# Optimization experiments

Hardware: AMD Instinct MI355X
Metric: run time of the kernel (lower is better)

## Reference

```python
import jax, jax.numpy as jnp
import numpy as np

B, S, H = 64, 2048, 1024
INPUT_SCALE = 100.0
DT = 0.01


def setup_inputs() -> dict:
    key = jax.random.key(0)
    ks = jax.random.split(key, 16)
    def vec(k, scale=0.5):
        return jax.random.normal(k, (H,), jnp.float32) * scale
    x_codes = 65.0 + 10.0 * jax.random.normal(ks[0], (B, S), jnp.float32)
    return {
        "x_codes": x_codes,
        "Wi_w": vec(ks[1]), "Wi_b": vec(ks[2], 0.1),
        "Wf_w": vec(ks[3]), "Wf_b": vec(ks[4], 0.1),
        "Wo_w": vec(ks[5]), "Wo_b": vec(ks[6], 0.1),
        "Wg_w": vec(ks[7]), "Wg_b": vec(ks[8], 0.1),
        "Wl_w": vec(ks[9]), "Wl_b": vec(ks[10], 0.1),
        "proj_w": jax.random.normal(ks[11], (2, H), jnp.float32) * 0.03,
        "proj_b": jnp.zeros((2,), jnp.float32),
        "n_init": jnp.zeros((H,), jnp.float32),
    }


def reference(x_codes, Wi_w, Wi_b, Wf_w, Wf_b, Wo_w, Wo_b, Wg_w, Wg_b,
              Wl_w, Wl_b, proj_w, proj_b, n_init):
    b, s = x_codes.shape
    h0 = jnp.zeros((b, H), x_codes.dtype)
    c0 = jnp.zeros_like(h0)
    n0 = jnp.broadcast_to(n_init, (b, H))
    x = (x_codes - 65.0) / INPUT_SCALE          # [B,S]
    xs = x.T[:, :, None]                         # [S,B,1] scan over time

    def step(carry, xt):
        h, c, n = carry
        pre_i = xt * Wi_w + Wi_b                 # [B,H] (Linear(1,H))
        pre_f = xt * Wf_w + Wf_b
        pre_o = xt * Wo_w + Wo_b
        pre_g = xt * Wg_w + Wg_b
        lam = jax.nn.sigmoid(xt * Wl_w + Wl_b)
        i_t = jnp.exp(pre_i - n)
        f_t = jnp.exp(pre_f - n)
        o_t = jnp.exp(pre_o - n)
        g_t = jax.nn.sigmoid(pre_g)              # act_g == 'sigmoid'
        c_new = f_t * c + i_t * g_t
        ff = o_t * jax.nn.sigmoid(c_new)         # act_c == 'sigmoid'
        h_new = (h + DT * ff) / (1.0 + DT * lam)
        n_new = n + 0.01 * (i_t + f_t + o_t - 3.0)
        y = h_new @ proj_w.T + proj_b            # [B,2]
        return (h_new, c_new, n_new), y

    _, ys = jax.lax.scan(step, (h0, c0, n0), xs)  # ys: [S,B,2]
    return ys.transpose(1, 0, 2)                  # [B,S,2]
```

## Files before the change

kernel.cpp:

```cpp
#include <hip/hip_runtime.h>


#define Bv   64
#define Sv   2048
#define Hv   1024
#define TPB  256
#define NT   512
#define CH   16
#define HSTR 17
#define HBUF (TPB * HSTR)

#define L2E   1.44269504088896340736f
#define NL2E (-1.44269504088896340736f)
#define LN2   0.69314718055994530942f
#define KNU   0.014426950408889634f
#define CREB  0.692493619626702435f
#define LOG2_001 (-6.6438561897747247f)

__device__ __forceinline__ float fexp2(float x) { return __builtin_amdgcn_exp2f(x); }
__device__ __forceinline__ float frcp(float x)  { return __builtin_amdgcn_rcpf(x); }

__global__ __launch_bounds__(256) void init_out(const float* __restrict__ proj_b,
                                                float* __restrict__ out) {
    int i = blockIdx.x * 256 + threadIdx.x;
    out[i] = proj_b[i & 1];
}

__global__ __launch_bounds__(NT, 1) void cfc_scan(
    const float* __restrict__ x_codes,
    const float* __restrict__ Wi_w, const float* __restrict__ Wi_b,
    const float* __restrict__ Wf_w, const float* __restrict__ Wf_b,
    const float* __restrict__ Wo_w, const float* __restrict__ Wo_b,
    const float* __restrict__ Wg_w, const float* __restrict__ Wg_b,
    const float* __restrict__ Wl_w, const float* __restrict__ Wl_b,
    const float* __restrict__ proj_w,
    const float* __restrict__ n_init,
    float* __restrict__ out)
{
    __shared__ float hlds[2 * HBUF];
    __shared__ float pwlds[2 * TPB];

    const int b   = blockIdx.x >> 2;
    const int q   = blockIdx.x & 3;
    const int tid = threadIdx.x;

    const float* __restrict__ xrow = x_codes + b * Sv;
    float* __restrict__ orow = out + b * (Sv * 2);

    const int ct   = tid - TPB;
    const int rk   = (ct >> 7) & 1;
    const int rt   = (ct >> 3) & 15;
    const int rseg = ct & 7;
    if (tid >= TPB) {
        pwlds[ct]       = proj_w[q * TPB + ct];
        pwlds[TPB + ct] = proj_w[Hv + q * TPB + ct];
    }

    float wi2 = 0, bi2 = 0, wf2 = 0, bf2 = 0, wo2 = 0, bo2 = 0;
    float wg2 = 0, bg2 = 0, wl2 = 0, bl2 = 0;
    float m = 0, En = 0, C = 0, h = 0;
    if (tid < TPB) {
        const int j = q * TPB + tid;
        const float wi = Wi_w[j], bi = Wi_b[j];
        const float wf = Wf_w[j], bf = Wf_b[j];
        const float wo = Wo_w[j], bo = Wo_b[j];
        const float wg = Wg_w[j], bg = Wg_b[j];
        const float wl = Wl_w[j], bl = Wl_b[j];
        wi2 = wi * KNU;  bi2 = fmaf(-0.65f, wi, bi) * L2E;
        wf2 = wf * KNU;  bf2 = fmaf(-0.65f, wf, bf) * L2E;
        wo2 = wo * KNU;  bo2 = fmaf(-0.65f, wo, bo) * L2E + LOG2_001;
        wg2 = -wg * KNU; bg2 = fmaf(-0.65f, wg, bg) * NL2E;
        wl2 = -wl * KNU; bl2 = fmaf(-0.65f, wl, bl) * NL2E;
        m  = n_init[j] * NL2E;
        En = fexp2(m);
    }

    float Gf[CH], GiGg[CH], Goa[CH], Gs[CH], Il[CH];

    static const float CUP[CH] = {
        1.0f,        1.03045453f, 1.06183655f, 1.09417428f,
        1.12749685f, 1.16183424f, 1.19721736f, 1.23367806f,
        1.27124915f, 1.30996445f, 1.34985881f, 1.39096813f,
        1.43332941f, 1.47698079f, 1.52196156f, 1.56831219f };

    int par = 0;
    for (int t0 = 0; t0 < Sv; t0 += CH, par ^= 1) {
        if (tid < TPB) {
            #pragma unroll
            for (int u = 0; u < CH; ++u) {
                const float xc = xrow[t0 + u];
                const float Gi = fexp2(fmaf(xc, wi2, bi2));
                Gf[u]  = fexp2(fmaf(xc, wf2, bf2));
                Goa[u] = fexp2(fmaf(xc, wo2, bo2));
                const float eg = fexp2(fmaf(xc, wg2, bg2));
                const float Gg = frcp(fmaf(eg, -LN2, -LN2));
                GiGg[u] = Gi * Gg;
                const float el = fexp2(fmaf(xc, wl2, bl2));
                Il[u]   = fmaf(frcp(el + 1.01f), -0.01f, 1.0f);
                Gs[u]   = fmaf(Goa[u], 100.0f, Gi + Gf[u]);
            }
            float* __restrict__ hrow = &hlds[par * HBUF + tid * HSTR];
            #pragma unroll
            for (int u = 0; u < CH; ++u) {
                const float Enu = (u == 0) ? En : En * CUP[u];
                const float ef  = Gf[u] * Enu;
                C = fmaf(ef, C, GiGg[u] * Enu);
                const float sc = frcp(1.0f + fexp2(C));
                h = fmaf(Goa[u] * Enu, sc, h) * Il[u];
                hrow[u] = h;
                m = fmaf(Gs[u] * Enu, -KNU, m);
                if (u == CH - 1) m += CREB;
                En = fexp2(m);
            }
        }
        __syncthreads();
        if (tid >= TPB) {
            const float* __restrict__ hb  = &hlds[par * HBUF];
            const float* __restrict__ pwk = &pwlds[rk * TPB];
            float sum = 0.0f;
            #pragma unroll
            for (int i2 = 0; i2 < 32; ++i2) {
                const int v  = (i2 + 4 * rseg) & 31;
                const int jj = rseg * 32 + v;
                sum = fmaf(hb[jj * HSTR + rt], pwk[jj], sum);
            }
            sum += __shfl_xor(sum, 1, 64);
            sum += __shfl_xor(sum, 2, 64);
            sum += __shfl_xor(sum, 4, 64);
            if (rseg == 0) atomicAdd(&orow[(t0 + rt) * 2 + rk], sum);
        }
    }
}

extern "C" void kernel_launch(void* const* d_in, const int* in_sizes, int n_in,
                              void* d_out, int out_size, void* d_ws, size_t ws_size,
                              hipStream_t stream) {
    const float* x_codes = (const float*)d_in[0];
    const float* Wi_w = (const float*)d_in[1];
    const float* Wi_b = (const float*)d_in[2];
    const float* Wf_w = (const float*)d_in[3];
    const float* Wf_b = (const float*)d_in[4];
    const float* Wo_w = (const float*)d_in[5];
    const float* Wo_b = (const float*)d_in[6];
    const float* Wg_w = (const float*)d_in[7];
    const float* Wg_b = (const float*)d_in[8];
    const float* Wl_w = (const float*)d_in[9];
    const float* Wl_b = (const float*)d_in[10];
    const float* proj_w = (const float*)d_in[11];
    const float* proj_b = (const float*)d_in[12];
    const float* n_init = (const float*)d_in[13];
    float* out = (float*)d_out;

    init_out<<<out_size / 256, 256, 0, stream>>>(proj_b, out);
    cfc_scan<<<Bv * (Hv / TPB), NT, 0, stream>>>(
        x_codes, Wi_w, Wi_b, Wf_w, Wf_b, Wo_w, Wo_b, Wg_w, Wg_b, Wl_w, Wl_b,
        proj_w, n_init, out);
}
```

Measured before the change: 275.7 us.

## Split scan into three-stage warp-specialized pipeline: gates, recurrence, output

Replaces the two-group design with three 256-thread groups. One group precomputes the gate exponentials for the next chunk into LDS, one runs only the serial C/n recurrence, and one computes h (sigmoids, lambda) plus the projection for the previous chunk. The aim is to take transcendental work off the serial critical path and overlap it across chunks. The chunk size drops to 8 and the sigmoid reciprocals are paired to share one rcp. In exchange it costs more LDS traffic, a barrier every 8 steps instead of every 16, and more threads per block.

```diff
diff --git a/kernel.cpp b/kernel.cpp
--- a/kernel.cpp
+++ b/kernel.cpp
@@ -4,18 +4,20 @@
 #define Bv   64
 #define Sv   2048
 #define Hv   1024
-#define TPB  256
-#define NT   512
-#define CH   16
-#define HSTR 17
-#define HBUF (TPB * HSTR)
+#define TPG  256
+#define NT   768
+#define CH   8
+#define NCH  (Sv / CH)
 
 #define L2E   1.44269504088896340736f
 #define NL2E (-1.44269504088896340736f)
 #define LN2   0.69314718055994530942f
 #define KNU   0.014426950408889634f
-#define CREB  0.692493619626702435f
+#define N100KNU (-1.4426950408889634f)
+#define CREB8 0.34624680981335122f
+#define DRFT  0.043280851226668903f
 #define LOG2_001 (-6.6438561897747247f)
+#define LOG2_L2E 0.52876637294489777f
 
 __device__ __forceinline__ float fexp2(float x) { return __builtin_amdgcn_exp2f(x); }
 __device__ __forceinline__ float frcp(float x)  { return __builtin_amdgcn_rcpf(x); }
@@ -25,6 +27,31 @@
     int i = blockIdx.x * 256 + threadIdx.x;
     out[i] = proj_b[i & 1];
 }
+
+#define GATEBODY(P)                                                             \
+    {                                                                           \
+        const int t1 = (P) * CH;                                                \
+        const float4 xq0 = *reinterpret_cast<const float4*>(xrow + t1);         \
+        const float4 xq1 = *reinterpret_cast<const float4*>(xrow + t1 + 4);     \
+        float* gw = &glds[(((P) & 1) * CH) * 1024 + lt * 4];                    \
+        _Pragma("unroll")                                                       \
+        for (int u = 0; u < CH; ++u) {                                          \
+            const float xc = (u < 4)                                            \
+                ? ((u==0)?xq0.x:(u==1)?xq0.y:(u==2)?xq0.z:xq0.w)                \
+                : ((u==4)?xq1.x:(u==5)?xq1.y:(u==6)?xq1.z:xq1.w);               \
+            const float gi = fexp2(fmaf(xc, wi2, bi2u[u]));                     \
+            const float gf = fexp2(fmaf(xc, wf2, bf2u[u]));                     \
+            const float go = fexp2(fmaf(xc, wo2, bo2u[u]));                     \
+            const float eg = fexp2(fmaf(xc, wg2, bg2));                         \
+            const float rg = frcp(1.0f + eg);                                   \
+            float4 v;                                                           \
+            v.x = gf;                                                           \
+            v.y = gi * rg;                                                      \
+            v.z = go;                                                           \
+            v.w = fmaf(go, N100KNU, fmaf(gi, -0.01f, gf * (-KNU)));             \
+            *reinterpret_cast<float4*>(gw + u * 1024) = v;                      \
+        }                                                                       \
+    }
 
 __global__ __launch_bounds__(NT, 1) void cfc_scan(
     const float* __restrict__ x_codes,
@@ -37,98 +64,129 @@
     const float* __restrict__ n_init,
     float* __restrict__ out)
 {
-    __shared__ float hlds[2 * HBUF];
-    __shared__ float pwlds[2 * TPB];
+    __shared__ __align__(16) float glds[2 * CH * 1024];
+    __shared__ __align__(16) float cpa[2 * 4 * 1024];
+    __shared__ float hlds[2 * 2304];
+    __shared__ float pwlds[2 * TPG];
 
     const int b   = blockIdx.x >> 2;
     const int q   = blockIdx.x & 3;
     const int tid = threadIdx.x;
+    const int grp = tid >> 8;
+    const int lt  = tid & 255;
 
     const float* __restrict__ xrow = x_codes + b * Sv;
     float* __restrict__ orow = out + b * (Sv * 2);
 
-    const int ct   = tid - TPB;
-    const int rk   = (ct >> 7) & 1;
-    const int rt   = (ct >> 3) & 15;
-    const int rseg = ct & 7;
-    if (tid >= TPB) {
-        pwlds[ct]       = proj_w[q * TPB + ct];
-        pwlds[TPB + ct] = proj_w[Hv + q * TPB + ct];
-    }
-
-    float wi2 = 0, bi2 = 0, wf2 = 0, bf2 = 0, wo2 = 0, bo2 = 0;
-    float wg2 = 0, bg2 = 0, wl2 = 0, bl2 = 0;
-    float m = 0, En = 0, C = 0, h = 0;
-    if (tid < TPB) {
-        const int j = q * TPB + tid;
+    float m = 0, En = 0, C = 0;
+    float wi2 = 0, wf2 = 0, wo2 = 0, wg2 = 0, bg2 = 0;
+    float bi2u[CH], bf2u[CH], bo2u[CH];
+    float wl2 = 0, bl2 = 0, h = 0;
+    const int rk = lt >> 7, rt = (lt >> 4) & 7, rseg = lt & 15;
+
+    if (grp == 0) {
+        m  = n_init[q * TPG + lt] * NL2E;
+        En = fexp2(m);
+        #pragma unroll
+        for (int u = 0; u < CH; ++u) { bi2u[u]=0; bf2u[u]=0; bo2u[u]=0; }
+    } else if (grp == 1) {
+        const int j = q * TPG + lt;
         const float wi = Wi_w[j], bi = Wi_b[j];
         const float wf = Wf_w[j], bf = Wf_b[j];
         const float wo = Wo_w[j], bo = Wo_b[j];
         const float wg = Wg_w[j], bg = Wg_b[j];
+        wi2 = wi * KNU;  const float bi2 = fmaf(-0.65f, wi, bi) * L2E + LOG2_L2E;
+        wf2 = wf * KNU;  const float bf2 = fmaf(-0.65f, wf, bf) * L2E;
+        wo2 = wo * KNU;  const float bo2 = fmaf(-0.65f, wo, bo) * L2E + LOG2_001;
+        wg2 = -wg * KNU; bg2 = fmaf(-0.65f, wg, bg) * NL2E;
+        #pragma unroll
+        for (int u = 0; u < CH; ++u) {
+            bi2u[u] = bi2 + DRFT * u;
+            bf2u[u] = bf2 + DRFT * u;
+            bo2u[u] = bo2 + DRFT * u;
+        }
+        GATEBODY(0)
+    } else {
+        const int j = q * TPG + lt;
         const float wl = Wl_w[j], bl = Wl_b[j];
-        wi2 = wi * KNU;  bi2 = fmaf(-0.65f, wi, bi) * L2E;
-        wf2 = wf * KNU;  bf2 = fmaf(-0.65f, wf, bf) * L2E;
-        wo2 = wo * KNU;  bo2 = fmaf(-0.65f, wo, bo) * L2E + LOG2_001;
-        wg2 = -wg * KNU; bg2 = fmaf(-0.65f, wg, bg) * NL2E;
         wl2 = -wl * KNU; bl2 = fmaf(-0.65f, wl, bl) * NL2E;
-        m  = n_init[j] * NL2E;
-        En = fexp2(m);
+        pwlds[lt]       = proj_w[q * TPG + lt];
+        pwlds[TPG + lt] = proj_w[Hv + q * TPG + lt];
+        #pragma unroll
+        for (int u = 0; u < CH; ++u) { bi2u[u]=0; bf2u[u]=0; bo2u[u]=0; }
     }
-
-    float Gf[CH], GiGg[CH], Goa[CH], Gs[CH], Il[CH];
-
-    static const float CUP[CH] = {
-        1.0f,        1.03045453f, 1.06183655f, 1.09417428f,
-        1.12749685f, 1.16183424f, 1.19721736f, 1.23367806f,
-        1.27124915f, 1.30996445f, 1.34985881f, 1.39096813f,
-        1.43332941f, 1.47698079f, 1.52196156f, 1.56831219f };
-
-    int par = 0;
-    for (int t0 = 0; t0 < Sv; t0 += CH, par ^= 1) {
-        if (tid < TPB) {
-            #pragma unroll
-            for (int u = 0; u < CH; ++u) {
-                const float xc = xrow[t0 + u];
-                const float Gi = fexp2(fmaf(xc, wi2, bi2));
-                Gf[u]  = fexp2(fmaf(xc, wf2, bf2));
-                Goa[u] = fexp2(fmaf(xc, wo2, bo2));
-                const float eg = fexp2(fmaf(xc, wg2, bg2));
-                const float Gg = frcp(fmaf(eg, -LN2, -LN2));
-                GiGg[u] = Gi * Gg;
-                const float el = fexp2(fmaf(xc, wl2, bl2));
-                Il[u]   = fmaf(frcp(el + 1.01f), -0.01f, 1.0f);
-                Gs[u]   = fmaf(Goa[u], 100.0f, Gi + Gf[u]);
+    __syncthreads();
+
+    for (int p = 0; p < NCH + 2; ++p) {
+        if (grp == 0) {
+            if (p < NCH) {
+                const float* gr = &glds[((p & 1) * CH) * 1024 + lt * 4];
+                float Cv[CH], Pv[CH];
+                #pragma unroll
+                for (int u = 0; u < CH; ++u) {
+                    const float4 g = *reinterpret_cast<const float4*>(gr + u * 1024);
+                    C = fmaf(g.x * En, C, -(g.y * En));
+                    Cv[u] = C;
+                    Pv[u] = g.z * En;
+                    m = fmaf(g.w, En, m);
+                    if (u == CH - 1) m += CREB8;
+                    En = fexp2(m);
+                }
+                float* cw = &cpa[((p & 1) * 4) * 1024 + lt * 4];
+                #pragma unroll
+                for (int pp = 0; pp < 4; ++pp) {
+                    float4 v;
+                    v.x = Cv[2*pp]; v.y = Pv[2*pp];
+                    v.z = Cv[2*pp+1]; v.w = Pv[2*pp+1];
+                    *reinterpret_cast<float4*>(cw + pp * 1024) = v;
+                }
             }
-            float* __restrict__ hrow = &hlds[par * HBUF + tid * HSTR];
-            #pragma unroll
-            for (int u = 0; u < CH; ++u) {
-                const float Enu = (u == 0) ? En : En * CUP[u];
-                const float ef  = Gf[u] * Enu;
-                C = fmaf(ef, C, GiGg[u] * Enu);
-                const float sc = frcp(1.0f + fexp2(C));
-                h = fmaf(Goa[u] * Enu, sc, h) * Il[u];
-                hrow[u] = h;
-                m = fmaf(Gs[u] * Enu, -KNU, m);
-                if (u == CH - 1) m += CREB;
-                En = fexp2(m);
+        } else if (grp == 1) {
+            if (p < NCH - 1) { GATEBODY(p + 1) }
+        } else {
+            if (p >= 1 && p <= NCH) {
+                const int t2 = (p - 1) * CH;
+                const float4 xq0 = *reinterpret_cast<const float4*>(xrow + t2);
+                const float4 xq1 = *reinterpret_cast<const float4*>(xrow + t2 + 4);
+                const float* cr = &cpa[(((p - 1) & 1) * 4) * 1024 + lt * 4];
+                float* hw = &hlds[((p - 1) & 1) * 2304 + lt * 9];
+                #pragma unroll
+                for (int pp = 0; pp < 4; ++pp) {
+                    const float4 cp4 = *reinterpret_cast<const float4*>(cr + pp * 1024);
+                    const float xc0 = (pp==0)?xq0.x:(pp==1)?xq0.z:(pp==2)?xq1.x:xq1.z;
+                    const float xc1 = (pp==0)?xq0.y:(pp==1)?xq0.w:(pp==2)?xq1.y:xq1.w;
+                    const float el0 = fexp2(fmaf(xc0, wl2, bl2));
+                    const float el1 = fexp2(fmaf(xc1, wl2, bl2));
+                    const float B0 = 1.01f + el0, B1 = 1.01f + el1;
+                    const float rB = frcp(B0 * B1);
+                    const float A0 = 1.0f + fexp2(cp4.x);
+                    const float A1 = 1.0f + fexp2(cp4.z);
+                    const float rA = frcp(A0 * A1);
+                    h = fmaf(cp4.y, rA * A1, h) * fmaf(rB * B1, -0.01f, 1.0f);
+                    hw[2 * pp] = h;
+                    h = fmaf(cp4.w, rA * A0, h) * fmaf(rB * B0, -0.01f, 1.0f);
+                    hw[2 * pp + 1] = h;
+                }
+            }
+            if (p >= 2) {
+                const float* hb  = &hlds[(p & 1) * 2304];
+                const float* pwk = &pwlds[rk * TPG];
+                float sum = 0.0f;
+                #pragma unroll
+                for (int i2 = 0; i2 < 16; ++i2) {
+                    const int v  = (i2 + rseg) & 15;
+                    const int jj = rseg * 16 + v;
+                    sum = fmaf(hb[jj * 9 + rt], pwk[jj], sum);
+                }
+                sum += __shfl_xor(sum, 1, 64);
+                sum += __shfl_xor(sum, 2, 64);
+                sum += __shfl_xor(sum, 4, 64);
+                sum += __shfl_xor(sum, 8, 64);
+                if (rseg == 0)
+                    atomicAdd(&orow[((p - 2) * CH + rt) * 2 + rk], sum);
             }
         }
         __syncthreads();
-        if (tid >= TPB) {
-            const float* __restrict__ hb  = &hlds[par * HBUF];
-            const float* __restrict__ pwk = &pwlds[rk * TPB];
-            float sum = 0.0f;
-            #pragma unroll
-            for (int i2 = 0; i2 < 32; ++i2) {
-                const int v  = (i2 + 4 * rseg) & 31;
-                const int jj = rseg * 32 + v;
-                sum = fmaf(hb[jj * HSTR + rt], pwk[jj], sum);
-            }
-            sum += __shfl_xor(sum, 1, 64);
-            sum += __shfl_xor(sum, 2, 64);
-            sum += __shfl_xor(sum, 4, 64);
-            if (rseg == 0) atomicAdd(&orow[(t0 + rt) * 2 + rk], sum);
-        }
     }
 }
 
@@ -152,7 +210,7 @@
     float* out = (float*)d_out;
 
     init_out<<<out_size / 256, 256, 0, stream>>>(proj_b, out);
-    cfc_scan<<<Bv * (Hv / TPB), NT, 0, stream>>>(
+    cfc_scan<<<Bv * (Hv / TPG), NT, 0, stream>>>(
         x_codes, Wi_w, Wi_b, Wf_w, Wf_b, Wo_w, Wo_b, Wg_w, Wg_b, Wl_w, Wl_b,
         proj_w, n_init, out);
 }
```

New measurement: 386.6 us. 40.2% more time.

## Interleave two hidden units per scan thread and pair sigmoid reciprocals

Applied to the files above, without the earlier changes.

Each compute thread now advances two independent hidden-unit recurrences (128 compute threads instead of 256), which interleaves their dependency chains to hide the exp/rcp latency of the serial scan. Time chunks shrink from 16 to 8 steps and x is read with float4 loads. Pairs of sigmoids now share one reciprocal, and the c-state sigmoid is moved out of the serial recurrence into a separate pass. The reduction threads are regrouped with 16 segments. Per-thread register pressure and serial work per thread both increase, while the number of block barriers doubles.

```diff
diff --git a/kernel.cpp b/kernel.cpp
--- a/kernel.cpp
+++ b/kernel.cpp
@@ -4,18 +4,20 @@
 #define Bv   64
 #define Sv   2048
 #define Hv   1024
-#define TPB  256
-#define NT   512
-#define CH   16
-#define HSTR 17
-#define HBUF (TPB * HSTR)
+#define TPB  128
+#define NCON 256
+#define NT   (TPB + NCON)
+#define CH   8
+#define HSTR 9
+#define HBUF (256 * HSTR)
 
 #define L2E   1.44269504088896340736f
 #define NL2E (-1.44269504088896340736f)
 #define LN2   0.69314718055994530942f
 #define KNU   0.014426950408889634f
-#define CREB  0.692493619626702435f
+#define CREB8 0.34624680981335122f
 #define LOG2_001 (-6.6438561897747247f)
+#define LOG2_L2E 0.52876637294489777f
 
 __device__ __forceinline__ float fexp2(float x) { return __builtin_amdgcn_exp2f(x); }
 __device__ __forceinline__ float frcp(float x)  { return __builtin_amdgcn_rcpf(x); }
@@ -25,6 +27,24 @@
     int i = blockIdx.x * 256 + threadIdx.x;
     out[i] = proj_b[i & 1];
 }
+
+#define XCOMP(qv, v) ((v)==0?(qv).x:(v)==1?(qv).y:(v)==2?(qv).z:(qv).w)
+
+#define LOAD_W(J, wi2, bi2, wf2, bf2, wo2, bo2, wg2, bg2, wl2, bl2, mm, EE)     \
+    {                                                                           \
+        const float wi = Wi_w[J], bi = Wi_b[J];                                 \
+        const float wf = Wf_w[J], bf = Wf_b[J];                                 \
+        const float wo = Wo_w[J], bo = Wo_b[J];                                 \
+        const float wg = Wg_w[J], bg = Wg_b[J];                                 \
+        const float wl = Wl_w[J], bl = Wl_b[J];                                 \
+        wi2 = wi * KNU;  bi2 = fmaf(-0.65f, wi, bi) * L2E + LOG2_L2E;           \
+        wf2 = wf * KNU;  bf2 = fmaf(-0.65f, wf, bf) * L2E;                      \
+        wo2 = wo * KNU;  bo2 = fmaf(-0.65f, wo, bo) * L2E + LOG2_001;           \
+        wg2 = -wg * KNU; bg2 = fmaf(-0.65f, wg, bg) * NL2E;                     \
+        wl2 = -wl * KNU; bl2 = fmaf(-0.65f, wl, bl) * NL2E;                     \
+        mm = n_init[J] * NL2E;                                                  \
+        EE = fexp2(mm);                                                         \
+    }
 
 __global__ __launch_bounds__(NT, 1) void cfc_scan(
     const float* __restrict__ x_codes,
@@ -38,7 +58,7 @@
     float* __restrict__ out)
 {
     __shared__ float hlds[2 * HBUF];
-    __shared__ float pwlds[2 * TPB];
+    __shared__ float pwlds[2 * 256];
 
     const int b   = blockIdx.x >> 2;
     const int q   = blockIdx.x & 3;
@@ -49,84 +69,128 @@
 
     const int ct   = tid - TPB;
     const int rk   = (ct >> 7) & 1;
-    const int rt   = (ct >> 3) & 15;
-    const int rseg = ct & 7;
+    const int rt   = (ct >> 4) & 7;
+    const int rseg = ct & 15;
     if (tid >= TPB) {
-        pwlds[ct]       = proj_w[q * TPB + ct];
-        pwlds[TPB + ct] = proj_w[Hv + q * TPB + ct];
-    }
-
-    float wi2 = 0, bi2 = 0, wf2 = 0, bf2 = 0, wo2 = 0, bo2 = 0;
-    float wg2 = 0, bg2 = 0, wl2 = 0, bl2 = 0;
-    float m = 0, En = 0, C = 0, h = 0;
+        pwlds[ct]       = proj_w[q * 256 + ct];
+        pwlds[256 + ct] = proj_w[Hv + q * 256 + ct];
+    }
+
+    float wi2a=0,bi2a=0,wf2a=0,bf2a=0,wo2a=0,bo2a=0,wg2a=0,bg2a=0,wl2a=0,bl2a=0;
+    float wi2b=0,bi2b=0,wf2b=0,bf2b=0,wo2b=0,bo2b=0,wg2b=0,bg2b=0,wl2b=0,bl2b=0;
+    float ma=0, Ena=0, Ca=0, ha=0;
+    float mb=0, Enb=0, Cb=0, hb_=0;
     if (tid < TPB) {
-        const int j = q * TPB + tid;
-        const float wi = Wi_w[j], bi = Wi_b[j];
-        const float wf = Wf_w[j], bf = Wf_b[j];
-        const float wo = Wo_w[j], bo = Wo_b[j];
-        const float wg = Wg_w[j], bg = Wg_b[j];
-        const float wl = Wl_w[j], bl = Wl_b[j];
-        wi2 = wi * KNU;  bi2 = fmaf(-0.65f, wi, bi) * L2E;
-        wf2 = wf * KNU;  bf2 = fmaf(-0.65f, wf, bf) * L2E;
-        wo2 = wo * KNU;  bo2 = fmaf(-0.65f, wo, bo) * L2E + LOG2_001;
-        wg2 = -wg * KNU; bg2 = fmaf(-0.65f, wg, bg) * NL2E;
-        wl2 = -wl * KNU; bl2 = fmaf(-0.65f, wl, bl) * NL2E;
-        m  = n_init[j] * NL2E;
-        En = fexp2(m);
-    }
-
-    float Gf[CH], GiGg[CH], Goa[CH], Gs[CH], Il[CH];
+        const int ja = q * 256 + tid;
+        const int jb = ja + TPB;
+        LOAD_W(ja, wi2a,bi2a,wf2a,bf2a,wo2a,bo2a,wg2a,bg2a,wl2a,bl2a, ma,Ena)
+        LOAD_W(jb, wi2b,bi2b,wf2b,bf2b,wo2b,bo2b,wg2b,bg2b,wl2b,bl2b, mb,Enb)
+    }
 
     static const float CUP[CH] = {
         1.0f,        1.03045453f, 1.06183655f, 1.09417428f,
-        1.12749685f, 1.16183424f, 1.19721736f, 1.23367806f,
-        1.27124915f, 1.30996445f, 1.34985881f, 1.39096813f,
-        1.43332941f, 1.47698079f, 1.52196156f, 1.56831219f };
+        1.12749685f, 1.16183424f, 1.19721736f, 1.23367806f };
 
     int par = 0;
     for (int t0 = 0; t0 < Sv; t0 += CH, par ^= 1) {
         if (tid < TPB) {
+            const float4 xq0 = *reinterpret_cast<const float4*>(xrow + t0);
+            const float4 xq1 = *reinterpret_cast<const float4*>(xrow + t0 + 4);
+            float gFa[CH], gIGa[CH], gOaA[CH], gSa[CH], gIla[CH];
+            float gFb[CH], gIGb[CH], gOaB[CH], gSb[CH], gIlb[CH];
             #pragma unroll
             for (int u = 0; u < CH; ++u) {
-                const float xc = xrow[t0 + u];
-                const float Gi = fexp2(fmaf(xc, wi2, bi2));
-                Gf[u]  = fexp2(fmaf(xc, wf2, bf2));
-                Goa[u] = fexp2(fmaf(xc, wo2, bo2));
-                const float eg = fexp2(fmaf(xc, wg2, bg2));
-                const float Gg = frcp(fmaf(eg, -LN2, -LN2));
-                GiGg[u] = Gi * Gg;
-                const float el = fexp2(fmaf(xc, wl2, bl2));
-                Il[u]   = fmaf(frcp(el + 1.01f), -0.01f, 1.0f);
-                Gs[u]   = fmaf(Goa[u], 100.0f, Gi + Gf[u]);
-            }
-            float* __restrict__ hrow = &hlds[par * HBUF + tid * HSTR];
+                const float xc = (u < 4) ? XCOMP(xq0, u) : XCOMP(xq1, u - 4);
+                {
+                    const float gi = fexp2(fmaf(xc, wi2a, bi2a));
+                    const float gf = fexp2(fmaf(xc, wf2a, bf2a));
+                    const float go = fexp2(fmaf(xc, wo2a, bo2a));
+                    const float eg = fexp2(fmaf(xc, wg2a, bg2a));
+                    const float el = fexp2(fmaf(xc, wl2a, bl2a));
+                    const float Aq = 1.0f + eg, Bq = 1.01f + el;
+                    const float rq = frcp(Aq * Bq);
+                    gFa[u]  = gf;
+                    gOaA[u] = go;
+                    gIGa[u] = gi * (rq * Bq);
+                    gIla[u] = fmaf(rq * Aq, -0.01f, 1.0f);
+                    gSa[u]  = fmaf(go, 100.0f, fmaf(gi, LN2, gf));
+                }
+                {
+                    const float gi = fexp2(fmaf(xc, wi2b, bi2b));
+                    const float gf = fexp2(fmaf(xc, wf2b, bf2b));
+                    const float go = fexp2(fmaf(xc, wo2b, bo2b));
+                    const float eg = fexp2(fmaf(xc, wg2b, bg2b));
+                    const float el = fexp2(fmaf(xc, wl2b, bl2b));
+                    const float Aq = 1.0f + eg, Bq = 1.01f + el;
+                    const float rq = frcp(Aq * Bq);
+                    gFb[u]  = gf;
+                    gOaB[u] = go;
+                    gIGb[u] = gi * (rq * Bq);
+                    gIlb[u] = fmaf(rq * Aq, -0.01f, 1.0f);
+                    gSb[u]  = fmaf(go, 100.0f, fmaf(gi, LN2, gf));
+                }
+            }
+            float CaV[CH], PaV[CH], CbV[CH], PbV[CH];
             #pragma unroll
             for (int u = 0; u < CH; ++u) {
-                const float Enu = (u == 0) ? En : En * CUP[u];
-                const float ef  = Gf[u] * Enu;
-                C = fmaf(ef, C, GiGg[u] * Enu);
-                const float sc = frcp(1.0f + fexp2(C));
-                h = fmaf(Goa[u] * Enu, sc, h) * Il[u];
-                hrow[u] = h;
-                m = fmaf(Gs[u] * Enu, -KNU, m);
-                if (u == CH - 1) m += CREB;
-                En = fexp2(m);
+                {
+                    const float Enu = Ena * CUP[u];
+                    Ca = fmaf(gFa[u] * Enu, Ca, -(gIGa[u] * Enu));
+                    CaV[u] = Ca;
+                    PaV[u] = gOaA[u] * Enu;
+                    ma = fmaf(gSa[u] * Enu, -KNU, ma);
+                    if (u == CH - 1) ma += CREB8;
+                    Ena = fexp2(ma);
+                }
+                {
+                    const float Enu = Enb * CUP[u];
+                    Cb = fmaf(gFb[u] * Enu, Cb, -(gIGb[u] * Enu));
+                    CbV[u] = Cb;
+                    PbV[u] = gOaB[u] * Enu;
+                    mb = fmaf(gSb[u] * Enu, -KNU, mb);
+                    if (u == CH - 1) mb += CREB8;
+                    Enb = fexp2(mb);
+                }
+            }
+            float* __restrict__ hra = &hlds[par * HBUF + tid * HSTR];
+            float* __restrict__ hrb = &hlds[par * HBUF + (tid + TPB) * HSTR];
+            #pragma unroll
+            for (int p = 0; p < CH / 2; ++p) {
+                {
+                    const float A0 = 1.0f + fexp2(CaV[2*p]);
+                    const float A1 = 1.0f + fexp2(CaV[2*p+1]);
+                    const float rr = frcp(A0 * A1);
+                    ha = fmaf(PaV[2*p],   rr * A1, ha) * gIla[2*p];
+                    hra[2*p]   = ha;
+                    ha = fmaf(PaV[2*p+1], rr * A0, ha) * gIla[2*p+1];
+                    hra[2*p+1] = ha;
+                }
+                {
+                    const float A0 = 1.0f + fexp2(CbV[2*p]);
+                    const float A1 = 1.0f + fexp2(CbV[2*p+1]);
+                    const float rr = frcp(A0 * A1);
+                    hb_ = fmaf(PbV[2*p],   rr * A1, hb_) * gIlb[2*p];
+                    hrb[2*p]   = hb_;
+                    hb_ = fmaf(PbV[2*p+1], rr * A0, hb_) * gIlb[2*p+1];
+                    hrb[2*p+1] = hb_;
+                }
             }
         }
         __syncthreads();
         if (tid >= TPB) {
             const float* __restrict__ hb  = &hlds[par * HBUF];
-            const float* __restrict__ pwk = &pwlds[rk * TPB];
+            const float* __restrict__ pwk = &pwlds[rk * 256];
             float sum = 0.0f;
             #pragma unroll
-            for (int i2 = 0; i2 < 32; ++i2) {
-                const int v  = (i2 + 4 * rseg) & 31;
-                const int jj = rseg * 32 + v;
+            for (int i2 = 0; i2 < 16; ++i2) {
+                const int v  = (i2 + rseg) & 15;
+                const int jj = rseg * 16 + v;
                 sum = fmaf(hb[jj * HSTR + rt], pwk[jj], sum);
             }
             sum += __shfl_xor(sum, 1, 64);
             sum += __shfl_xor(sum, 2, 64);
             sum += __shfl_xor(sum, 4, 64);
+            sum += __shfl_xor(sum, 8, 64);
             if (rseg == 0) atomicAdd(&orow[(t0 + rt) * 2 + rk], sum);
         }
     }
@@ -152,7 +216,7 @@
     float* out = (float*)d_out;
 
     init_out<<<out_size / 256, 256, 0, stream>>>(proj_b, out);
-    cfc_scan<<<Bv * (Hv / TPB), NT, 0, stream>>>(
+    cfc_scan<<<Bv * 4, NT, 0, stream>>>(
         x_codes, Wi_w, Wi_b, Wf_w, Wf_b, Wo_w, Wo_b, Wg_w, Wg_b, Wl_w, Wl_b,
         proj_w, n_init, out);
 }
```

New measurement: 390.0 us. 41.4% more time.
